# Optimization experiments

Hardware: AMD Instinct MI355X
Metric: run time of the kernel (lower is better)

## Reference

```python
import jax, jax.numpy as jnp
import numpy as np

N = 50000      # num nodes
E = 800000     # num edges
D = 128        # num_hid
EPS = 1e-8


def _mlp(x, w1, b1, w2, b2):
    # 2-layer MLP: Linear -> ReLU -> Linear (dropout disabled at inference)
    return jax.nn.relu(x @ w1 + b1) @ w2 + b2


def setup_inputs() -> dict:
    key = jax.random.key(0)
    ks = jax.random.split(key, 12)

    def lin(k, fan_in, fan_out):
        kw, kb = jax.random.split(k)
        lim = 1.0 / np.sqrt(fan_in)
        w = jax.random.uniform(kw, (fan_in, fan_out), jnp.float32, -lim, lim)
        b = jax.random.uniform(kb, (fan_out,), jnp.float32, -lim, lim)
        return w, b

    H = jax.random.normal(ks[0], (N, D), jnp.float32)
    edge_index = jax.random.randint(ks[1], (2, E), 0, N, jnp.int64)
    w1_1, b1_1 = lin(ks[2], 2 * D, D)   # mlp_1 layer 1
    w1_2, b1_2 = lin(ks[3], D, D)       # mlp_1 layer 2
    w2_1, b2_1 = lin(ks[4], 2 * D, D)   # mlp_2 layer 1
    w2_2, b2_2 = lin(ks[5], D, 1)       # mlp_2 layer 2 (channel_curv=False -> out=1)
    t = jnp.zeros((), jnp.float32)
    return {"t": t, "H": H, "edge_index": edge_index,
            "w1_1": w1_1, "b1_1": b1_1, "w1_2": w1_2, "b1_2": b1_2,
            "w2_1": w2_1, "b2_1": b2_1, "w2_2": w2_2, "b2_2": b2_2}


def reference(t, H, edge_index, w1_1, b1_1, w1_2, b1_2, w2_1, b2_1, w2_2, b2_2):
    src, dst = edge_index[0], edge_index[1]

    # damping: row-normalize H
    H = H / (jnp.linalg.norm(H, axis=1, keepdims=True) + EPS)

    H_i = H[src]                                    # [E, D]
    H_j = H[dst]                                    # [E, D]

    # curvature(H_i, H_j)
    c = jnp.concatenate((H_i, H_j), axis=1)         # [E, 2D]
    c = jax.nn.relu(_mlp(c, w1_1, b1_1, w1_2, b1_2))  # [E, D]
    c = jax.ops.segment_sum(c, src, num_segments=N)   # scatter-sum -> [N, D]
    c = jnp.concatenate((c[src], c[dst]), axis=1)     # [E, 2D]
    curv = _mlp(c, w2_1, b2_1, w2_2, b2_2)            # [E, 1]

    # damped edge message
    cos = jnp.sum(H_i * H_j, axis=1, keepdims=True)   # [E, 1]
    H_edge = curv * (H_j - cos * H_i)                 # [E, D]

    # scatter-mean over source node
    s = jax.ops.segment_sum(H_edge, src, num_segments=N)               # [N, D]
    cnt = jax.ops.segment_sum(jnp.ones((E, 1), H.dtype), src, num_segments=N)
    Hm = s / jnp.maximum(cnt, 1.0)

    # damping: row-normalize output
    return Hm / (jnp.linalg.norm(Hm, axis=1, keepdims=True) + EPS)
```

## Files before the change

### kernel.cpp

```cpp
#include <hip/hip_runtime.h>
#include <hip/hip_bf16.h>

#define D 128
#define EPS 1e-8f
#define E1S 136

typedef _Float16 f16;
typedef __attribute__((ext_vector_type(8))) _Float16 half8;
typedef __attribute__((ext_vector_type(4))) float f32x4;
typedef unsigned int uint;

__device__ inline float2 up2(uint u) {
    union { uint u; f16 h[2]; } v; v.u = u;
    return make_float2((float)v.h[0], (float)v.h[1]);
}

__global__ void k_prologue(const float* __restrict__ H, f16* __restrict__ HT,
                           const int* __restrict__ src, int* __restrict__ deg,
                           const float* __restrict__ w1_1, const float* __restrict__ w1_2,
                           const float* __restrict__ w2_1, f16* __restrict__ Wt,
                           int N, int E, int nbN) {
    int b = blockIdx.x;
    int t = threadIdx.x;
    if (b < nbN) {
        int row = b * 4 + (t >> 6);
        int lane = t & 63;
        if (row >= N) return;
        float2 v = reinterpret_cast<const float2*>(H + (size_t)row * D)[lane];
        float ss = v.x * v.x + v.y * v.y;
        #pragma unroll
        for (int off = 32; off; off >>= 1) ss += __shfl_xor(ss, off, 64);
        float scale = 1.0f / (sqrtf(ss) + EPS);
        union { f16 h[2]; uint u; } p;
        p.h[0] = (f16)(v.x * scale);
        p.h[1] = (f16)(v.y * scale);
        reinterpret_cast<uint*>(HT + (size_t)row * 256)[lane] = p.u;
    } else if (b < nbN + 1024) {
        int bb = b - nbN;
        for (int e = bb * 256 + t; e < E; e += 1024 * 256)
            atomicAdd(&deg[src[e]], 1);
    } else {
        int bb = b - nbN - 1024;
        int m = bb >> 6;
        int idx = (bb & 63) * 256 + t;
        int k = idx >> 7, n = idx & 127;
        const float* W = (m == 0) ? w1_1
                       : (m == 1) ? w1_1 + 16384
                       : (m == 2) ? w1_2
                       : (m == 3) ? w2_1
                                  : w2_1 + 16384;
        Wt[m * 16384 + n * 128 + k] = (f16)W[k * 128 + n];
    }
}

__global__ void k_scan(const int* __restrict__ deg, int* __restrict__ rowptr, int N) {
    __shared__ int wsum[16];
    __shared__ int carry;
    int t = threadIdx.x, lane = t & 63, w = t >> 6;
    if (t == 0) carry = 0;
    __syncthreads();
    for (int base = 0; base < N; base += 4096) {
        int i0 = base + t * 4;
        int a = 0, b = 0, c = 0, d = 0;
        if (i0 + 3 < N) {
            int4 v4 = *reinterpret_cast<const int4*>(deg + i0);
            a = v4.x; b = v4.y; c = v4.z; d = v4.w;
        } else {
            if (i0 < N) a = deg[i0];
            if (i0 + 1 < N) b = deg[i0 + 1];
            if (i0 + 2 < N) c = deg[i0 + 2];
            if (i0 + 3 < N) d = deg[i0 + 3];
        }
        int s1 = a + b, s2 = s1 + c, s3 = s2 + d;
        int v = s3;
        #pragma unroll
        for (int off = 1; off < 64; off <<= 1) {
            int u = __shfl_up(v, off, 64);
            if (lane >= off) v += u;
        }
        if (lane == 63) wsum[w] = v;
        __syncthreads();
        if (w == 0 && lane < 16) {
            int s = wsum[lane];
            #pragma unroll
            for (int off = 1; off < 16; off <<= 1) {
                int u = __shfl_up(s, off, 64);
                if (lane >= off) s += u;
            }
            wsum[lane] = s;
        }
        __syncthreads();
        int add = (w > 0 ? wsum[w - 1] : 0) + carry;
        int incl = v + add;
        int pre = incl - s3;
        if (i0 < N)     rowptr[i0 + 1] = pre + a;
        if (i0 + 1 < N) rowptr[i0 + 2] = pre + s1;
        if (i0 + 2 < N) rowptr[i0 + 3] = pre + s2;
        if (i0 + 3 < N) rowptr[i0 + 4] = pre + s3;
        __syncthreads();
        if (t == 1023) carry = incl;
        __syncthreads();
    }
    if (t == 0) rowptr[0] = 0;
}

__global__ void k_scatter(const int* __restrict__ src, const int* __restrict__ dst,
                          const int* __restrict__ rowptr, int* __restrict__ fill,
                          int* __restrict__ srcS, int* __restrict__ dstS, int E) {
    for (int e = blockIdx.x * blockDim.x + threadIdx.x; e < E; e += gridDim.x * blockDim.x) {
        int s = src[e];
        int pos = atomicAdd(&fill[s], 1);
        int idx = rowptr[s] + pos;
        srcS[idx] = s;
        dstS[idx] = dst[e];
    }
}

template <bool A_F16>
__global__ __launch_bounds__(256, 4)
void k_gemm_dual(const void* __restrict__ Aptr, const f16* __restrict__ Wt0,
                 const f16* __restrict__ Wt1, const float* __restrict__ bias0,
                 f16* __restrict__ out0, f16* __restrict__ out1, int N,
                 int astr, int o1str) {
    __shared__ f16 As[64 * E1S];
    int t = threadIdx.x;
    int r0 = blockIdx.x * 64;
    int l = t & 63, w = t >> 6, n0 = w * 32;
    {
        int er = t >> 2, kb = (t & 3) * 32;
        int rc = min(r0 + er, N - 1);
        if (A_F16) {
            const half8* Ap = reinterpret_cast<const half8*>((const f16*)Aptr + (size_t)rc * astr + kb);
            #pragma unroll
            for (int q = 0; q < 4; ++q)
                *reinterpret_cast<half8*>(&As[er * E1S + kb + q * 8]) = Ap[q];
        } else {
            const float4* Ap = reinterpret_cast<const float4*>((const float*)Aptr + (size_t)rc * astr + kb);
            #pragma unroll
            for (int q = 0; q < 4; ++q) {
                float4 a0 = Ap[q * 2], a1 = Ap[q * 2 + 1];
                half8 sv;
                sv[0] = (f16)a0.x; sv[1] = (f16)a0.y; sv[2] = (f16)a0.z; sv[3] = (f16)a0.w;
                sv[4] = (f16)a1.x; sv[5] = (f16)a1.y; sv[6] = (f16)a1.z; sv[7] = (f16)a1.w;
                *reinterpret_cast<half8*>(&As[er * E1S + kb + q * 8]) = sv;
            }
        }
    }
    half8 bfrag[2][4];
    #pragma unroll
    for (int nt = 0; nt < 2; ++nt) {
        int col = n0 + nt * 16 + (l & 15);
        #pragma unroll
        for (int kt = 0; kt < 4; ++kt)
            bfrag[nt][kt] = *reinterpret_cast<const half8*>(Wt0 + col * 128 + kt * 32 + (l >> 4) * 8);
    }
    float b0a = bias0[n0 + (l & 15)];
    float b0b = bias0[n0 + 16 + (l & 15)];
    __syncthreads();
    f32x4 acc0[4][2], acc1[4][2];
    #pragma unroll
    for (int mt = 0; mt < 4; ++mt) {
        acc0[mt][0] = (f32x4){0,0,0,0}; acc0[mt][1] = (f32x4){0,0,0,0};
        acc1[mt][0] = (f32x4){0,0,0,0}; acc1[mt][1] = (f32x4){0,0,0,0};
    }
    #pragma unroll
    for (int mt = 0; mt < 4; ++mt) {
        int arow = mt * 16 + (l & 15);
        #pragma unroll
        for (int kt = 0; kt < 4; ++kt) {
            half8 af = *reinterpret_cast<const half8*>(&As[arow * E1S + kt * 32 + (l >> 4) * 8]);
            acc0[mt][0] = __builtin_amdgcn_mfma_f32_16x16x32_f16(af, bfrag[0][kt], acc0[mt][0], 0, 0, 0);
            acc0[mt][1] = __builtin_amdgcn_mfma_f32_16x16x32_f16(af, bfrag[1][kt], acc0[mt][1], 0, 0, 0);
        }
    }
    #pragma unroll
    for (int nt = 0; nt < 2; ++nt) {
        int col = n0 + nt * 16 + (l & 15);
        #pragma unroll
        for (int kt = 0; kt < 4; ++kt)
            bfrag[nt][kt] = *reinterpret_cast<const half8*>(Wt1 + col * 128 + kt * 32 + (l >> 4) * 8);
    }
    #pragma unroll
    for (int mt = 0; mt < 4; ++mt) {
        int arow = mt * 16 + (l & 15);
        #pragma unroll
        for (int kt = 0; kt < 4; ++kt) {
            half8 af = *reinterpret_cast<const half8*>(&As[arow * E1S + kt * 32 + (l >> 4) * 8]);
            acc1[mt][0] = __builtin_amdgcn_mfma_f32_16x16x32_f16(af, bfrag[0][kt], acc1[mt][0], 0, 0, 0);
            acc1[mt][1] = __builtin_amdgcn_mfma_f32_16x16x32_f16(af, bfrag[1][kt], acc1[mt][1], 0, 0, 0);
        }
    }
    __syncthreads();
    #pragma unroll
    for (int mt = 0; mt < 4; ++mt)
        #pragma unroll
        for (int j = 0; j < 4; ++j) {
            int row = mt * 16 + (l >> 4) * 4 + j;
            As[row * E1S + n0 + (l & 15)]      = (f16)(acc0[mt][0][j] + b0a);
            As[row * E1S + n0 + 16 + (l & 15)] = (f16)(acc0[mt][1][j] + b0b);
        }
    __syncthreads();
    {
        int er = t >> 2, kb = (t & 3) * 32;
        int row = r0 + er;
        if (row < N)
            #pragma unroll
            for (int q = 0; q < 4; ++q)
                *reinterpret_cast<half8*>(out0 + (size_t)row * 128 + kb + q * 8) =
                    *reinterpret_cast<const half8*>(&As[er * E1S + kb + q * 8]);
    }
    __syncthreads();
    #pragma unroll
    for (int mt = 0; mt < 4; ++mt)
        #pragma unroll
        for (int j = 0; j < 4; ++j) {
            int row = mt * 16 + (l >> 4) * 4 + j;
            As[row * E1S + n0 + (l & 15)]      = (f16)acc1[mt][0][j];
            As[row * E1S + n0 + 16 + (l & 15)] = (f16)acc1[mt][1][j];
        }
    __syncthreads();
    {
        int er = t >> 2, kb = (t & 3) * 32;
        int row = r0 + er;
        if (row < N)
            #pragma unroll
            for (int q = 0; q < 4; ++q)
                *reinterpret_cast<half8*>(out1 + (size_t)row * o1str + kb + q * 8) =
                    *reinterpret_cast<const half8*>(&As[er * E1S + kb + q * 8]);
    }
}

__global__ __launch_bounds__(256, 5)
void k_edge_mlp1(const int* __restrict__ srcS, const int* __restrict__ dstS,
                 const int* __restrict__ rowptr,
                 const f16* __restrict__ P, const f16* __restrict__ Q,
                 const f16* __restrict__ Wt, const float* __restrict__ b1_2,
                 float* __restrict__ C, int E) {
    __shared__ f16 e1s[64 * E1S];
    int t = threadIdx.x;
    int e0 = blockIdx.x * 64;
    int l = t & 63, w = t >> 6, n0 = w * 32;
    {
        int er = t >> 2, kb = (t & 3) * 32;
        int ge = min(e0 + er, E - 1);
        int sc = srcS[ge], dj = dstS[ge];
        const half8* Pp = reinterpret_cast<const half8*>(P + (size_t)sc * 128 + kb);
        const half8* Qp = reinterpret_cast<const half8*>(Q + (size_t)dj * 128 + kb);
        #pragma unroll
        for (int q = 0; q < 4; ++q) {
            half8 sv = Pp[q] + Qp[q];
            #pragma unroll
            for (int i = 0; i < 8; ++i)
                sv[i] = sv[i] > (f16)0 ? sv[i] : (f16)0;
            *reinterpret_cast<half8*>(&e1s[er * E1S + kb + q * 8]) = sv;
        }
    }
    half8 bfrag[2][4];
    #pragma unroll
    for (int nt = 0; nt < 2; ++nt) {
        int col = n0 + nt * 16 + (l & 15);
        #pragma unroll
        for (int kt = 0; kt < 4; ++kt)
            bfrag[nt][kt] = *reinterpret_cast<const half8*>(Wt + col * 128 + kt * 32 + (l >> 4) * 8);
    }
    float bias0 = b1_2[n0 + (l & 15)];
    float bias1 = b1_2[n0 + 16 + (l & 15)];
    __syncthreads();
    f32x4 acc[4][2];
    #pragma unroll
    for (int mt = 0; mt < 4; ++mt) { acc[mt][0] = (f32x4){0,0,0,0}; acc[mt][1] = (f32x4){0,0,0,0}; }
    #pragma unroll
    for (int mt = 0; mt < 4; ++mt) {
        int arow = mt * 16 + (l & 15);
        #pragma unroll
        for (int kt = 0; kt < 4; ++kt) {
            half8 af = *reinterpret_cast<const half8*>(&e1s[arow * E1S + kt * 32 + (l >> 4) * 8]);
            acc[mt][0] = __builtin_amdgcn_mfma_f32_16x16x32_f16(af, bfrag[0][kt], acc[mt][0], 0, 0, 0);
            acc[mt][1] = __builtin_amdgcn_mfma_f32_16x16x32_f16(af, bfrag[1][kt], acc[mt][1], 0, 0, 0);
        }
    }
    #pragma unroll
    for (int mt = 0; mt < 4; ++mt)
        #pragma unroll
        for (int j = 0; j < 4; ++j) {
            acc[mt][0][j] = fmaxf(acc[mt][0][j] + bias0, 0.f);
            acc[mt][1][j] = fmaxf(acc[mt][1][j] + bias1, 0.f);
        }
    int myv = (e0 + l < E) ? srcS[e0 + l] : -1;
    int pv = __shfl_up(myv, 1, 64);
    bool head = (l == 0) || (myv != pv);
    unsigned long long validm = __ballot(myv >= 0);
    unsigned long long hm = __ballot(head) & validm;
    int nvalid = __popcll(validm);
    int grp = l >> 4;
    while (hm) {
        int lo = __builtin_ctzll(hm);
        hm &= hm - 1;
        int hi = hm ? __builtin_ctzll(hm) : nvalid;
        int s = __shfl(myv, lo, 64);
        float v0 = 0.f, v1 = 0.f;
        #pragma unroll
        for (int mt = 0; mt < 4; ++mt) {
            int tlo = mt * 16, thi = mt * 16 + 16;
            if (thi <= lo || tlo >= hi) continue;
            if (lo <= tlo && hi >= thi) {
                #pragma unroll
                for (int j = 0; j < 4; ++j) {
                    v0 += acc[mt][0][j];
                    v1 += acc[mt][1][j];
                }
            } else {
                #pragma unroll
                for (int j = 0; j < 4; ++j) {
                    int row = tlo + grp * 4 + j;
                    bool in = (row >= lo) && (row < hi);
                    v0 += in ? acc[mt][0][j] : 0.f;
                    v1 += in ? acc[mt][1][j] : 0.f;
                }
            }
        }
        v0 += __shfl_xor(v0, 16, 64); v0 += __shfl_xor(v0, 32, 64);
        v1 += __shfl_xor(v1, 16, 64); v1 += __shfl_xor(v1, 32, 64);
        if (l < 16) {
            int rs = rowptr[s], re = rowptr[s + 1];
            float* cp = C + (size_t)s * 128 + n0 + l;
            if (rs >= e0 && re <= e0 + 64) {
                cp[0] = v0; cp[16] = v1;
            } else {
                atomicAdd(cp, v0); atomicAdd(cp + 16, v1);
            }
        }
    }
}

__global__ void k_node_curv(const int* __restrict__ dstS, const int* __restrict__ rowptr,
                            const f16* __restrict__ HT, const f16* __restrict__ Rb,
                            const float* __restrict__ w2_2, const float* __restrict__ b2_2,
                            float* __restrict__ out, int N) {
    int node = blockIdx.x * 4 + (threadIdx.x >> 6);
    int lane = threadIdx.x & 63;
    if (node >= N) return;
    int sub = lane & 15;
    int slot = lane >> 4;
    const uint4* HTU = reinterpret_cast<const uint4*>(HT);
    uint4 hiu = HTU[(size_t)node * 32 + sub];
    uint4 rvu = reinterpret_cast<const uint4*>(Rb)[(size_t)node * 16 + sub];
    float hif[8], rvf[8], wvf[8];
    {
        const uint* hp = &hiu.x;
        const uint* rp = &rvu.x;
        float4 w0 = reinterpret_cast<const float4*>(w2_2)[sub * 2];
        float4 w1 = reinterpret_cast<const float4*>(w2_2)[sub * 2 + 1];
        #pragma unroll
        for (int k = 0; k < 4; ++k) {
            float2 h = up2(hp[k]); hif[k * 2] = h.x; hif[k * 2 + 1] = h.y;
            float2 r = up2(rp[k]); rvf[k * 2] = r.x; rvf[k * 2 + 1] = r.y;
        }
        wvf[0] = w0.x; wvf[1] = w0.y; wvf[2] = w0.z; wvf[3] = w0.w;
        wvf[4] = w1.x; wvf[5] = w1.y; wvf[6] = w1.z; wvf[7] = w1.w;
    }
    float bb = b2_2[0];
    int lo = rowptr[node], hiE = rowptr[node + 1];
    int deg = hiE - lo;
    float ax[8];
    #pragma unroll
    for (int j = 0; j < 8; ++j) ax[j] = 0.f;
    float sc = 0.f;
    int e = lo + slot;
    bool valid = e < hiE;
    int dcur = valid ? dstS[e] : 0;
    uint4 hju = HTU[(size_t)dcur * 32 + sub];
    uint4 tvu = HTU[(size_t)dcur * 32 + 16 + sub];
    for (int it = 0; it < deg; it += 4) {
        int e2 = lo + it + 4 + slot;
        bool valid2 = e2 < hiE;
        int d2 = valid2 ? dstS[e2] : 0;
        uint4 hjN = HTU[(size_t)d2 * 32 + sub];
        uint4 tvN = HTU[(size_t)d2 * 32 + 16 + sub];
        float hjf[8];
        float pcos = 0.f, pcur = 0.f;
        {
            const uint* hp = &hju.x;
            const uint* tp = &tvu.x;
            #pragma unroll
            for (int k = 0; k < 4; ++k) {
                float2 h = up2(hp[k]);
                float2 tv = up2(tp[k]);
                hjf[k * 2] = h.x; hjf[k * 2 + 1] = h.y;
                pcos += hif[k * 2] * h.x + hif[k * 2 + 1] * h.y;
                pcur += fmaxf(rvf[k * 2] + tv.x, 0.f) * wvf[k * 2]
                      + fmaxf(rvf[k * 2 + 1] + tv.y, 0.f) * wvf[k * 2 + 1];
            }
        }
        #pragma unroll
        for (int off = 1; off < 16; off <<= 1) {
            pcos += __shfl_xor(pcos, off, 64);
            pcur += __shfl_xor(pcur, off, 64);
        }
        float cur = valid ? (pcur + bb) : 0.f;
        #pragma unroll
        for (int j = 0; j < 8; ++j) ax[j] += cur * hjf[j];
        sc += cur * pcos;
        hju = hjN; tvu = tvN; valid = valid2;
    }
    #pragma unroll
    for (int j = 0; j < 8; ++j) {
        ax[j] += __shfl_xor(ax[j], 16, 64);
        ax[j] += __shfl_xor(ax[j], 32, 64);
    }
    sc += __shfl_xor(sc, 16, 64);
    sc += __shfl_xor(sc, 32, 64);
    float inv = 1.0f / fmaxf((float)deg, 1.0f);
    float ss = 0.f;
    #pragma unroll
    for (int j = 0; j < 8; ++j) {
        ax[j] = (ax[j] - sc * hif[j]) * inv;
        ss += ax[j] * ax[j];
    }
    #pragma unroll
    for (int off = 1; off < 16; off <<= 1) ss += __shfl_xor(ss, off, 64);
    float scale = 1.0f / (sqrtf(ss) + EPS);
    if (slot == 0) {
        float4 o0 = make_float4(ax[0] * scale, ax[1] * scale, ax[2] * scale, ax[3] * scale);
        float4 o1 = make_float4(ax[4] * scale, ax[5] * scale, ax[6] * scale, ax[7] * scale);
        float4* op = reinterpret_cast<float4*>(out + (size_t)node * 128 + sub * 8);
        op[0] = o0;
        op[1] = o1;
    }
}

extern "C" void kernel_launch(void* const* d_in, const int* in_sizes, int n_in,
                              void* d_out, int out_size, void* d_ws, size_t ws_size,
                              hipStream_t stream) {
    const float* H    = (const float*)d_in[1];
    const int*   ei   = (const int*)d_in[2];
    const float* w1_1 = (const float*)d_in[3];
    const float* b1_1 = (const float*)d_in[4];
    const float* w1_2 = (const float*)d_in[5];
    const float* b1_2 = (const float*)d_in[6];
    const float* w2_1 = (const float*)d_in[7];
    const float* b2_1 = (const float*)d_in[8];
    const float* w2_2 = (const float*)d_in[9];
    const float* b2_2 = (const float*)d_in[10];

    int N = in_sizes[1] / D;
    int E = in_sizes[2] / 2;
    const int* src = ei;
    const int* dst = ei + E;

    float* out = (float*)d_out;

    f16* HT     = (f16*)d_ws;
    f16* Pb     = HT + (size_t)N * 256;
    f16* Qb     = Pb + (size_t)N * D;
    float* Cb   = (float*)(Qb + (size_t)N * D);
    f16* Wt     = (f16*)(Cb + (size_t)N * D);
    int* deg    = (int*)(Wt + 5 * 16384);
    int* rowptr = deg + N;
    int* fill   = rowptr + N + 1;
    int* srcS   = fill + N;
    int* dstS   = srcS + E;

    hipMemsetAsync(Cb, 0, (size_t)N * D * sizeof(float), stream);
    hipMemsetAsync(deg, 0, (3 * (size_t)N + 1) * sizeof(int), stream);

    int nbN = (N + 3) / 4;
    k_prologue<<<nbN + 1024 + 320, 256, 0, stream>>>(H, HT, src, deg,
                                                     w1_1, w1_2, w2_1, Wt, N, E, nbN);
    k_scan<<<1, 1024, 0, stream>>>(deg, rowptr, N);
    k_scatter<<<1024, 256, 0, stream>>>(src, dst, rowptr, fill, srcS, dstS, E);

    k_gemm_dual<true><<<(N + 63) / 64, 256, 0, stream>>>(HT, Wt + 0 * 16384, Wt + 1 * 16384,
                                                         b1_1, Pb, Qb, N, 256, 128);
    k_edge_mlp1<<<(E + 63) / 64, 256, 0, stream>>>(srcS, dstS, rowptr, Pb, Qb,
                                                   Wt + 2 * 16384, b1_2, Cb, E);
    k_gemm_dual<false><<<(N + 63) / 64, 256, 0, stream>>>(Cb, Wt + 3 * 16384, Wt + 4 * 16384,
                                                          b2_1, Pb, HT + 128, N, 128, 256);
    k_node_curv<<<(N + 3) / 4, 256, 0, stream>>>(dstS, rowptr, HT, Pb, w2_2, b2_2, out, N);
}
```

Measured before the change: 345.9 us.

## Make edge MLP kernel persistent and stage unique source rows in LDS

The edge MLP kernel becomes a persistent grid-stride loop over 64-edge tiles on a fixed 1280-block grid, so the weight fragments are loaded into registers once per block instead of once per tile. Within each tile, edges are grouped by their sorted source node: a wave-level prefix scan numbers the unique sources, and each unique P row is loaded once into shared memory and reused by every edge with that source. Tiles with more than 32 unique sources fall back to direct global loads. The new path adds extra LDS (about 8.7KB plus index arrays) and more barriers per tile, which may reduce occupancy under the 5-blocks launch bound. With about 16 edges per node on average, a tile usually has only a few unique sources, so the redundant P reads were already probably served from cache.

```diff
diff --git a/kernel.cpp b/kernel.cpp
--- a/kernel.cpp
+++ b/kernel.cpp
@@ -4,6 +4,7 @@
 #define D 128
 #define EPS 1e-8f
 #define E1S 136
+#define PS  136
 
 typedef _Float16 f16;
 typedef __attribute__((ext_vector_type(8))) _Float16 half8;
@@ -235,26 +236,15 @@
                  const int* __restrict__ rowptr,
                  const f16* __restrict__ P, const f16* __restrict__ Q,
                  const f16* __restrict__ Wt, const float* __restrict__ b1_2,
-                 float* __restrict__ C, int E) {
+                 float* __restrict__ C, int E, int ntiles) {
     __shared__ f16 e1s[64 * E1S];
+    __shared__ f16 Pstage[32 * PS];
+    __shared__ int ssrc_l[64], sdst_l[64], pslot_l[64], hsrc_l[64];
+    __shared__ int nh_l;
     int t = threadIdx.x;
-    int e0 = blockIdx.x * 64;
     int l = t & 63, w = t >> 6, n0 = w * 32;
-    {
-        int er = t >> 2, kb = (t & 3) * 32;
-        int ge = min(e0 + er, E - 1);
-        int sc = srcS[ge], dj = dstS[ge];
-        const half8* Pp = reinterpret_cast<const half8*>(P + (size_t)sc * 128 + kb);
-        const half8* Qp = reinterpret_cast<const half8*>(Q + (size_t)dj * 128 + kb);
-        #pragma unroll
-        for (int q = 0; q < 4; ++q) {
-            half8 sv = Pp[q] + Qp[q];
-            #pragma unroll
-            for (int i = 0; i < 8; ++i)
-                sv[i] = sv[i] > (f16)0 ? sv[i] : (f16)0;
-            *reinterpret_cast<half8*>(&e1s[er * E1S + kb + q * 8]) = sv;
-        }
-    }
+    int er = t >> 2, kb = (t & 3) * 32;
+
     half8 bfrag[2][4];
     #pragma unroll
     for (int nt = 0; nt < 2; ++nt) {
@@ -265,69 +255,123 @@
     }
     float bias0 = b1_2[n0 + (l & 15)];
     float bias1 = b1_2[n0 + 16 + (l & 15)];
-    __syncthreads();
-    f32x4 acc[4][2];
-    #pragma unroll
-    for (int mt = 0; mt < 4; ++mt) { acc[mt][0] = (f32x4){0,0,0,0}; acc[mt][1] = (f32x4){0,0,0,0}; }
-    #pragma unroll
-    for (int mt = 0; mt < 4; ++mt) {
-        int arow = mt * 16 + (l & 15);
-        #pragma unroll
-        for (int kt = 0; kt < 4; ++kt) {
-            half8 af = *reinterpret_cast<const half8*>(&e1s[arow * E1S + kt * 32 + (l >> 4) * 8]);
-            acc[mt][0] = __builtin_amdgcn_mfma_f32_16x16x32_f16(af, bfrag[0][kt], acc[mt][0], 0, 0, 0);
-            acc[mt][1] = __builtin_amdgcn_mfma_f32_16x16x32_f16(af, bfrag[1][kt], acc[mt][1], 0, 0, 0);
-        }
-    }
-    #pragma unroll
-    for (int mt = 0; mt < 4; ++mt)
-        #pragma unroll
-        for (int j = 0; j < 4; ++j) {
-            acc[mt][0][j] = fmaxf(acc[mt][0][j] + bias0, 0.f);
-            acc[mt][1][j] = fmaxf(acc[mt][1][j] + bias1, 0.f);
-        }
-    int myv = (e0 + l < E) ? srcS[e0 + l] : -1;
-    int pv = __shfl_up(myv, 1, 64);
-    bool head = (l == 0) || (myv != pv);
-    unsigned long long validm = __ballot(myv >= 0);
-    unsigned long long hm = __ballot(head) & validm;
-    int nvalid = __popcll(validm);
-    int grp = l >> 4;
-    while (hm) {
-        int lo = __builtin_ctzll(hm);
-        hm &= hm - 1;
-        int hi = hm ? __builtin_ctzll(hm) : nvalid;
-        int s = __shfl(myv, lo, 64);
-        float v0 = 0.f, v1 = 0.f;
+
+    for (int tile = blockIdx.x; tile < ntiles; tile += gridDim.x) {
+        int e0 = tile * 64;
+        __syncthreads();
+        if (t < 64) {
+            int ge = min(e0 + t, E - 1);
+            int s0 = srcS[ge];
+            ssrc_l[t] = s0;
+            sdst_l[t] = dstS[ge];
+            int sp = __shfl_up(s0, 1, 64);
+            int head = (t == 0 || s0 != sp) ? 1 : 0;
+            int incl = head;
+            #pragma unroll
+            for (int off = 1; off < 64; off <<= 1) {
+                int u = __shfl_up(incl, off, 64);
+                if (t >= off) incl += u;
+            }
+            pslot_l[t] = incl - 1;
+            if (head) hsrc_l[incl - 1] = s0;
+            if (t == 63) nh_l = incl;
+        }
+        __syncthreads();
+        int nh = nh_l;
+        if (nh <= 32) {
+            for (int i = t; i < nh * 16; i += 256) {
+                int slot = i >> 4, ch = i & 15;
+                *reinterpret_cast<half8*>(&Pstage[slot * PS + ch * 8]) =
+                    *reinterpret_cast<const half8*>(P + (size_t)hsrc_l[slot] * 128 + ch * 8);
+            }
+        }
+        __syncthreads();
+        {
+            int dj = sdst_l[er];
+            const half8* Qp = reinterpret_cast<const half8*>(Q + (size_t)dj * 128 + kb);
+            half8 p[4];
+            if (nh <= 32) {
+                const half8* Pp = reinterpret_cast<const half8*>(&Pstage[pslot_l[er] * PS + kb]);
+                #pragma unroll
+                for (int q = 0; q < 4; ++q) p[q] = Pp[q];
+            } else {
+                const half8* Pp = reinterpret_cast<const half8*>(P + (size_t)ssrc_l[er] * 128 + kb);
+                #pragma unroll
+                for (int q = 0; q < 4; ++q) p[q] = Pp[q];
+            }
+            #pragma unroll
+            for (int q = 0; q < 4; ++q) {
+                half8 sv = p[q] + Qp[q];
+                #pragma unroll
+                for (int i = 0; i < 8; ++i)
+                    sv[i] = sv[i] > (f16)0 ? sv[i] : (f16)0;
+                *reinterpret_cast<half8*>(&e1s[er * E1S + kb + q * 8]) = sv;
+            }
+        }
+        __syncthreads();
+        f32x4 acc[4][2];
+        #pragma unroll
+        for (int mt = 0; mt < 4; ++mt) { acc[mt][0] = (f32x4){0,0,0,0}; acc[mt][1] = (f32x4){0,0,0,0}; }
         #pragma unroll
         for (int mt = 0; mt < 4; ++mt) {
-            int tlo = mt * 16, thi = mt * 16 + 16;
-            if (thi <= lo || tlo >= hi) continue;
-            if (lo <= tlo && hi >= thi) {
-                #pragma unroll
-                for (int j = 0; j < 4; ++j) {
-                    v0 += acc[mt][0][j];
-                    v1 += acc[mt][1][j];
+            int arow = mt * 16 + (l & 15);
+            #pragma unroll
+            for (int kt = 0; kt < 4; ++kt) {
+                half8 af = *reinterpret_cast<const half8*>(&e1s[arow * E1S + kt * 32 + (l >> 4) * 8]);
+                acc[mt][0] = __builtin_amdgcn_mfma_f32_16x16x32_f16(af, bfrag[0][kt], acc[mt][0], 0, 0, 0);
+                acc[mt][1] = __builtin_amdgcn_mfma_f32_16x16x32_f16(af, bfrag[1][kt], acc[mt][1], 0, 0, 0);
+            }
+        }
+        #pragma unroll
+        for (int mt = 0; mt < 4; ++mt)
+            #pragma unroll
+            for (int j = 0; j < 4; ++j) {
+                acc[mt][0][j] = fmaxf(acc[mt][0][j] + bias0, 0.f);
+                acc[mt][1][j] = fmaxf(acc[mt][1][j] + bias1, 0.f);
+            }
+        int myv = (e0 + l < E) ? ssrc_l[l] : -1;
+        int pv = __shfl_up(myv, 1, 64);
+        bool head = (l == 0) || (myv != pv);
+        unsigned long long validm = __ballot(myv >= 0);
+        unsigned long long hm = __ballot(head) & validm;
+        int nvalid = __popcll(validm);
+        int grp = l >> 4;
+        while (hm) {
+            int lo = __builtin_ctzll(hm);
+            hm &= hm - 1;
+            int hi = hm ? __builtin_ctzll(hm) : nvalid;
+            int s = __shfl(myv, lo, 64);
+            float v0 = 0.f, v1 = 0.f;
+            #pragma unroll
+            for (int mt = 0; mt < 4; ++mt) {
+                int tlo = mt * 16, thi = mt * 16 + 16;
+                if (thi <= lo || tlo >= hi) continue;
+                if (lo <= tlo && hi >= thi) {
+                    #pragma unroll
+                    for (int j = 0; j < 4; ++j) {
+                        v0 += acc[mt][0][j];
+                        v1 += acc[mt][1][j];
+                    }
+                } else {
+                    #pragma unroll
+                    for (int j = 0; j < 4; ++j) {
+                        int row = tlo + grp * 4 + j;
+                        bool in = (row >= lo) && (row < hi);
+                        v0 += in ? acc[mt][0][j] : 0.f;
+                        v1 += in ? acc[mt][1][j] : 0.f;
+                    }
                 }
-            } else {
-                #pragma unroll
-                for (int j = 0; j < 4; ++j) {
-                    int row = tlo + grp * 4 + j;
-                    bool in = (row >= lo) && (row < hi);
-                    v0 += in ? acc[mt][0][j] : 0.f;
-                    v1 += in ? acc[mt][1][j] : 0.f;
+            }
+            v0 += __shfl_xor(v0, 16, 64); v0 += __shfl_xor(v0, 32, 64);
+            v1 += __shfl_xor(v1, 16, 64); v1 += __shfl_xor(v1, 32, 64);
+            if (l < 16) {
+                int rs = rowptr[s], re = rowptr[s + 1];
+                float* cp = C + (size_t)s * 128 + n0 + l;
+                if (rs >= e0 && re <= e0 + 64) {
+                    cp[0] = v0; cp[16] = v1;
+                } else {
+                    atomicAdd(cp, v0); atomicAdd(cp + 16, v1);
                 }
-            }
-        }
-        v0 += __shfl_xor(v0, 16, 64); v0 += __shfl_xor(v0, 32, 64);
-        v1 += __shfl_xor(v1, 16, 64); v1 += __shfl_xor(v1, 32, 64);
-        if (l < 16) {
-            int rs = rowptr[s], re = rowptr[s + 1];
-            float* cp = C + (size_t)s * 128 + n0 + l;
-            if (rs >= e0 && re <= e0 + 64) {
-                cp[0] = v0; cp[16] = v1;
-            } else {
-                atomicAdd(cp, v0); atomicAdd(cp + 16, v1);
             }
         }
     }
@@ -470,10 +514,11 @@
     k_scan<<<1, 1024, 0, stream>>>(deg, rowptr, N);
     k_scatter<<<1024, 256, 0, stream>>>(src, dst, rowptr, fill, srcS, dstS, E);
 
+    int ntiles = (E + 63) / 64;
     k_gemm_dual<true><<<(N + 63) / 64, 256, 0, stream>>>(HT, Wt + 0 * 16384, Wt + 1 * 16384,
                                                          b1_1, Pb, Qb, N, 256, 128);
-    k_edge_mlp1<<<(E + 63) / 64, 256, 0, stream>>>(srcS, dstS, rowptr, Pb, Qb,
-                                                   Wt + 2 * 16384, b1_2, Cb, E);
+    k_edge_mlp1<<<1280, 256, 0, stream>>>(srcS, dstS, rowptr, Pb, Qb,
+                                          Wt + 2 * 16384, b1_2, Cb, E, ntiles);
     k_gemm_dual<false><<<(N + 63) / 64, 256, 0, stream>>>(Cb, Wt + 3 * 16384, Wt + 4 * 16384,
                                                           b2_1, Pb, HT + 128, N, 128, 256);
     k_node_curv<<<(N + 3) / 4, 256, 0, stream>>>(dstS, rowptr, HT, Pb, w2_2, b2_2, out, N);
```

After: 389.1 us. 12.5% more time.
